# Kernel optimization log

Measured on AMD Instinct MI355X. Metric: run time of the kernel, lower is better.

Reference implementation:

```python
import jax, jax.numpy as jnp
import numpy as np

EMBED_DIM = 2048
NUM_HEADS = 32
NUM_KV_HEADS = 8
HEAD_DIM = EMBED_DIM // NUM_HEADS  # 64
KV_DIM = HEAD_DIM * NUM_KV_HEADS   # 512
ROPE_BASE = 10000.0


def rope_cos_sin(seq_len, dim):
    inv_freq = 1.0 / (ROPE_BASE ** (jnp.arange(0, dim, 2, dtype=jnp.float32) / dim))
    t = jnp.arange(seq_len, dtype=jnp.float32)
    freqs = jnp.outer(t, inv_freq)                 # [T, dim/2]
    emb = jnp.concatenate([freqs, freqs], axis=-1)  # [T, dim]
    return jnp.cos(emb), jnp.sin(emb)


def rotate_half(x):
    half = x.shape[-1] // 2
    return jnp.concatenate([-x[..., half:], x[..., :half]], axis=-1)


def setup_inputs() -> dict:
    key = jax.random.key(0)
    k_x, k_q, k_k, k_v, k_o = jax.random.split(key, 5)
    B, T, C = 2, 2048, EMBED_DIM
    s = 1.0 / np.sqrt(C)
    x = jax.random.normal(k_x, (B, T, C), dtype=jnp.float32)
    # Linear weights stored as [in, out]; no bias (bias=False)
    Wq = jax.random.normal(k_q, (C, EMBED_DIM), dtype=jnp.float32) * s
    Wk = jax.random.normal(k_k, (C, KV_DIM), dtype=jnp.float32) * s
    Wv = jax.random.normal(k_v, (C, KV_DIM), dtype=jnp.float32) * s
    Wo = jax.random.normal(k_o, (C, EMBED_DIM), dtype=jnp.float32) * s
    return {"x": x, "Wq": Wq, "Wk": Wk, "Wv": Wv, "Wo": Wo}


def reference(x, Wq, Wk, Wv, Wo):
    B, T, C = x.shape
    H, KVH, D = NUM_HEADS, NUM_KV_HEADS, HEAD_DIM
    scale = D ** -0.5
    rep = H // KVH

    q = (x @ Wq).reshape(B, T, H, D).transpose(0, 2, 1, 3)    # [B,H,T,D]
    k = (x @ Wk).reshape(B, T, KVH, D).transpose(0, 2, 1, 3)  # [B,KVH,T,D]
    v = (x @ Wv).reshape(B, T, KVH, D).transpose(0, 2, 1, 3)
    # repeat_interleave over head dim to expand KV heads
    k = jnp.repeat(k, rep, axis=1)  # [B,H,T,D]
    v = jnp.repeat(v, rep, axis=1)

    cos, sin = rope_cos_sin(T, D)
    cos = cos[None, None, :, :]
    sin = sin[None, None, :, :]
    q = q * cos + rotate_half(q) * sin
    k = k * cos + rotate_half(k) * sin

    att = jnp.einsum('bhtd,bhsd->bhts', q, k) * scale  # [B,H,T,T]
    att = jax.nn.softmax(att, axis=-1)                 # mask=None, dropout eval
    y = jnp.einsum('bhts,bhsd->bhtd', att, v)          # [B,H,T,D]
    y = y.transpose(0, 2, 1, 3).reshape(B, T, C)
    return y @ Wo
```

## Files before the change

kernel.cpp:

```cpp
#include <hip/hip_runtime.h>
#include <stdint.h>

#define Tn   2048
#define Cn   2048
#define Hn   32
#define KVHn 8
#define Dn   64
#define MR   4096
#define NQKV 3072
#define KD   2048

typedef __attribute__((ext_vector_type(4))) float fx4;
typedef __attribute__((ext_vector_type(8))) short frag8;

#define MFMA(a,b,c) __builtin_amdgcn_mfma_f32_16x16x32_bf16((a),(b),(c),0,0,0)

struct __align__(16) U16x8 { unsigned short s[8]; };

__device__ __forceinline__ unsigned short f2bf(float x){
  union { float f; unsigned u; } v; v.f = x;
  return (unsigned short)((v.u + 0x7FFFu + ((v.u >> 16) & 1u)) >> 16);
}
__device__ __forceinline__ float bf2f(unsigned short h){
  union { unsigned u; float f; } v; v.u = ((unsigned)h) << 16; return v.f;
}
__device__ __forceinline__ float sexp2(float x){
#if __has_builtin(__builtin_amdgcn_exp2f)
  return __builtin_amdgcn_exp2f(x);
#else
  return exp2f(x);
#endif
}
__device__ __forceinline__ unsigned cvtpk(float a, float b){
  unsigned r; asm("v_cvt_pk_bf16_f32 %0, %1, %2" : "=v"(r) : "v"(a), "v"(b)); return r;
}

typedef const __attribute__((address_space(1))) void cas1_void;
typedef __attribute__((address_space(3))) void as3_void;
__device__ __forceinline__ void gld16(const void* g, void* l){
  __builtin_amdgcn_global_load_lds((cas1_void*)g, (as3_void*)l, 16, 0, 0);
}

__global__ __launch_bounds__(256) void k_prep(const float* __restrict__ x, unsigned short* __restrict__ xb,
                                              const float* __restrict__ Wq, const float* __restrict__ Wk,
                                              const float* __restrict__ Wv, unsigned short* __restrict__ wqkvt,
                                              const float* __restrict__ Wo, unsigned short* __restrict__ wot,
                                              float2* __restrict__ cs){
  __shared__ float tile[64][65];
  int blk = blockIdx.x, t = threadIdx.x;
  if (blk < 2048) {
    size_t blockbase = (size_t)blk * 4096;
    #pragma unroll
    for (int j = 0; j < 4; ++j) {
      size_t i = blockbase + j * 1024 + t * 4;
      float4 v = *(const float4*)(x + i);
      ushort4 o; o.x = f2bf(v.x); o.y = f2bf(v.y); o.z = f2bf(v.z); o.w = f2bf(v.w);
      *(ushort4*)(xb + i) = o;
    }
    return;
  }
  if (blk >= 4608) {
    int i = (blk - 4608) * 256 + t;
    int tp = i >> 5, d = i & 31;
    float inv = powf(10000.0f, -(float)d * (1.0f/32.0f));
    float fr = (float)tp * inv;
    cs[i] = make_float2(cosf(fr), sinf(fr));
    return;
  }
  const float* src; int col0, ld, n0, k0; unsigned short* outp;
  if (blk < 3584) {
    int bx = blk - 2048; n0 = (bx % 48) * 64; k0 = (bx / 48) * 64; outp = wqkvt;
    if (n0 < 2048)      { src = Wq; col0 = n0;        ld = 2048; }
    else if (n0 < 2560) { src = Wk; col0 = n0 - 2048; ld = 512;  }
    else                { src = Wv; col0 = n0 - 2560; ld = 512;  }
  } else {
    int bx = blk - 3584; n0 = (bx % 32) * 64; k0 = (bx / 32) * 64; outp = wot;
    src = Wo; col0 = n0; ld = 2048;
  }
  int r = t >> 2, cc = (t & 3) << 4;
  const float* p = src + (size_t)(k0 + r) * ld + col0 + cc;
  #pragma unroll
  for (int j = 0; j < 16; j += 4) {
    float4 v = *(const float4*)(p + j);
    tile[r][cc + j + 0] = v.x; tile[r][cc + j + 1] = v.y;
    tile[r][cc + j + 2] = v.z; tile[r][cc + j + 3] = v.w;
  }
  __syncthreads();
  int n = t >> 2, kc = (t & 3) << 4;
  unsigned short* q = outp + (size_t)(n0 + n) * 2048 + k0 + kc;
  U16x8 o0, o1;
  #pragma unroll
  for (int j = 0; j < 8; ++j) o0.s[j] = f2bf(tile[kc + j][n]);
  #pragma unroll
  for (int j = 0; j < 8; ++j) o1.s[j] = f2bf(tile[kc + 8 + j][n]);
  *(U16x8*)(q) = o0;
  *(U16x8*)(q + 8) = o1;
}

template<int MODE>
__global__ __launch_bounds__(256) void k_gemm(const unsigned short* __restrict__ A,
                                              const unsigned short* __restrict__ Bt,
                                              void* __restrict__ Cp,
                                              int M, int N, int K,
                                              const float2* __restrict__ cs){
  __shared__ unsigned short As[128 * 64];
  __shared__ unsigned short Bs[128 * 64];
  int tid = threadIdx.x;
  int m0 = blockIdx.y * 128, n0 = blockIdx.x * 128;
  int w = tid >> 6, ln = tid & 63, lr = ln & 15, lg = ln >> 4;
  int wm = (w >> 1) * 64, wn = (w & 1) * 64;
  fx4 acc[4][4];
  #pragma unroll
  for (int i = 0; i < 4; ++i)
    #pragma unroll
    for (int j = 0; j < 4; ++j) acc[i][j] = (fx4){0.f,0.f,0.f,0.f};
  int steps = K >> 6;
  for (int kt = 0; kt < steps; ++kt) {
    int kb = kt << 6;
    #pragma unroll
    for (int it = 0; it < 4; ++it) {
      int nch = it * 256 + tid;
      int r = nch >> 3, c = (nch & 7) ^ (r & 7);
      gld16(A  + (size_t)(m0 + r) * K + kb + c * 8, (char*)As + nch * 16);
      gld16(Bt + (size_t)(n0 + r) * K + kb + c * 8, (char*)Bs + nch * 16);
    }
    __syncthreads();
    frag8 aF[4][2], bF[4][2];
    #pragma unroll
    for (int i = 0; i < 4; ++i) {
      int ra = wm + i * 16 + lr;
      int rb = wn + i * 16 + lr;
      #pragma unroll
      for (int kk = 0; kk < 2; ++kk) {
        aF[i][kk] = *(const frag8*)((const char*)As + ra * 128 + (((lg + 4*kk) ^ (ra & 7)) << 4));
        bF[i][kk] = *(const frag8*)((const char*)Bs + rb * 128 + (((lg + 4*kk) ^ (rb & 7)) << 4));
      }
    }
    #pragma unroll
    for (int kk = 0; kk < 2; ++kk)
      #pragma unroll
      for (int i = 0; i < 4; ++i)
        #pragma unroll
        for (int j = 0; j < 4; ++j)
          acc[i][j] = MFMA(aF[i][kk], bF[j][kk], acc[i][j]);
    __syncthreads();
  }
  if (MODE == 0) {
    #pragma unroll
    for (int i = 0; i < 4; ++i) {
      int row = m0 + wm + i * 16 + lg * 4;
      #pragma unroll
      for (int j = 0; j < 4; ++j) {
        int col = n0 + wn + j * 16 + lr;
        #pragma unroll
        for (int rr = 0; rr < 4; ++rr)
          ((float*)Cp)[(size_t)(row + rr) * N + col] = acc[i][j][rr];
      }
    }
  } else {
    int nb = n0 + wn;
    unsigned short* outp = (unsigned short*)Cp;
    if (nb < 2560) {
      float sc = (n0 < 2048) ? 0.180336880f : 1.0f;
      #pragma unroll
      for (int i = 0; i < 4; ++i) {
        int rowb = m0 + wm + i * 16 + lg * 4;
        #pragma unroll
        for (int jp = 0; jp < 2; ++jp) {
          int dA = jp * 16 + lr;
          #pragma unroll
          for (int rr = 0; rr < 4; ++rr) {
            int row = rowb + rr;
            float2 cv = cs[((row & (Tn-1)) << 5) + dA];
            float a = acc[i][jp][rr], b = acc[i][jp + 2][rr];
            outp[(size_t)row * N + nb + dA]      = f2bf((a * cv.x - b * cv.y) * sc);
            outp[(size_t)row * N + nb + dA + 32] = f2bf((b * cv.x + a * cv.y) * sc);
          }
        }
      }
    } else {
      #pragma unroll
      for (int i = 0; i < 4; ++i) {
        int row = m0 + wm + i * 16 + lg * 4;
        #pragma unroll
        for (int j = 0; j < 4; ++j) {
          int col = nb + j * 16 + lr;
          #pragma unroll
          for (int rr = 0; rr < 4; ++rr)
            outp[(size_t)(row + rr) * N + col] = f2bf(acc[i][j][rr]);
        }
      }
    }
  }
}

__global__ __launch_bounds__(256) void k_vt(const unsigned short* __restrict__ qkv,
                                            unsigned short* __restrict__ vt){
  __shared__ unsigned short tl[64][66];
  int head = blockIdx.y;
  int b = head >> 3, kvh = head & 7;
  int t0 = blockIdx.x * 64;
  int t = threadIdx.x;
  int r = t >> 2, cc = (t & 3) << 4;
  const unsigned short* p = qkv + (size_t)(b * Tn + t0 + r) * NQKV + 2560 + kvh * 64 + cc;
  U16x8 v0 = *(const U16x8*)(p);
  U16x8 v1 = *(const U16x8*)(p + 8);
  #pragma unroll
  for (int j = 0; j < 8; ++j) { tl[r][cc + j] = v0.s[j]; tl[r][cc + 8 + j] = v1.s[j]; }
  __syncthreads();
  int d = t >> 2, cpair = t & 3;
  unsigned short* q = vt + ((size_t)head * 64 + d) * Tn + t0;
  #pragma unroll
  for (int ci = 0; ci < 2; ++ci) {
    int c = cpair * 2 + ci;
    U16x8 oo;
    #pragma unroll
    for (int e = 0; e < 8; ++e)
      oo.s[e] = tl[32 * (c >> 2) + 16 * (e >> 2) + 4 * (c & 3) + (e & 3)][d];
    *(U16x8*)(q + c * 8) = oo;
  }
}

__global__ __launch_bounds__(512) void k_attn(const unsigned short* __restrict__ qkv,
                                              const unsigned short* __restrict__ vt,
                                              unsigned short* __restrict__ y){
  __shared__ unsigned short Ks[4][64 * 64];
  __shared__ unsigned short Vs[4][64 * 64];
  int tid = threadIdx.x, w = tid >> 6, ln = tid & 63, lq = ln & 15, lg = ln >> 4;
  int bh = blockIdx.y, b = bh >> 5, h = bh & 31, kvh = h >> 2;
  int q0 = blockIdx.x * 256;
  frag8 qF[2][2];
  #pragma unroll
  for (int s = 0; s < 2; ++s) {
    const unsigned short* qrow = qkv + (size_t)(b * Tn + q0 + w * 32 + 16 * s + lq) * NQKV + h * 64;
    qF[s][0] = *(const frag8*)(qrow + lg * 8);
    qF[s][1] = *(const frag8*)(qrow + 32 + lg * 8);
  }
  fx4 zero4 = (fx4){0.f, 0.f, 0.f, 0.f};
  asm volatile("" : "+v"(zero4));
  int n0 = tid;
  int r0 = n0 >> 3, c0 = (n0 & 7) ^ (r0 & 7);
  const unsigned short* kp0 = qkv + (size_t)b * Tn * NQKV + 2048 + kvh * 64 + (size_t)r0 * NQKV + c0 * 8;
  const unsigned short* vp0 = vt + ((size_t)(b * 8 + kvh) * 64 + r0) * Tn + c0 * 8;
  int koff0 = lq * 128 + (((lg)     ^ (lq & 7)) << 4);
  int koff1 = lq * 128 + (((lg + 4) ^ (lq & 7)) << 4);

#define STAGE(BUF) do {                                      \
    gld16(kp0, (char*)&Ks[BUF][0] + n0 * 16);                \
    gld16(vp0, (char*)&Vs[BUF][0] + n0 * 16);                \
    kp0 += 64 * NQKV; vp0 += 64;                             \
  } while (0)

#define PB(S, KK) ({ union { unsigned u[4]; frag8 f; } t_;                        \
    t_.u[0] = pu[S][2*(KK)][0]; t_.u[1] = pu[S][2*(KK)][1];                       \
    t_.u[2] = pu[S][2*(KK)+1][0]; t_.u[3] = pu[S][2*(KK)+1][1]; t_.f; })

#define PVSTEP(VF) do {                                                           \
    _Pragma("unroll")                                                             \
    for (int s = 0; s < 2; ++s)                                                   \
      _Pragma("unroll")                                                           \
      for (int df = 0; df < 4; ++df) {                                            \
        o[s][df] = MFMA(VF[df][0], PB(s, 0), o[s][df]);                           \
        o[s][df] = MFMA(VF[df][1], PB(s, 1), o[s][df]);                           \
      }                                                                           \
  } while (0)

#define TILE(BUF, VFCUR, VFPREV) do {                                             \
    const char* kb_ = (const char*)&Ks[BUF][0];                                   \
    const char* vb_ = (const char*)&Vs[BUF][0];                                   \
    frag8 kf[4][2];                                                               \
    _Pragma("unroll")                                                             \
    for (int mf = 0; mf < 4; ++mf) {                                              \
      kf[mf][0] = *(const frag8*)(kb_ + mf * 2048 + koff0);                       \
      kf[mf][1] = *(const frag8*)(kb_ + mf * 2048 + koff1);                       \
    }                                                                             \
    _Pragma("unroll")                                                             \
    for (int df = 0; df < 4; ++df) {                                              \
      VFCUR[df][0] = *(const frag8*)(vb_ + df * 2048 + koff0);                    \
      VFCUR[df][1] = *(const frag8*)(vb_ + df * 2048 + koff1);                    \
    }                                                                             \
    __builtin_amdgcn_s_setprio(1);                                                \
    PVSTEP(VFPREV);                       \
    fx4 sf[2][4];                                                                 \
    _Pragma("unroll")                                                             \
    for (int s = 0; s < 2; ++s)                                                   \
      _Pragma("unroll")                                                           \
      for (int mf = 0; mf < 4; ++mf) {                                            \
        sf[s][mf] = MFMA(kf[mf][0], qF[s][0], zero4);                             \
        sf[s][mf] = MFMA(kf[mf][1], qF[s][1], sf[s][mf]);                         \
      }                                                                           \
    __builtin_amdgcn_s_setprio(0);                                                \
    _Pragma("unroll")                                \
    for (int s = 0; s < 2; ++s) {                                                 \
      float ps = 0.f;                                                             \
      _Pragma("unroll")                                                           \
      for (int mf = 0; mf < 4; ++mf) {                                            \
        float p0 = sexp2(sf[s][mf][0]);                                           \
        float p1 = sexp2(sf[s][mf][1]);                                           \
        float p2 = sexp2(sf[s][mf][2]);                                           \
        float p3 = sexp2(sf[s][mf][3]);                                           \
        ps += (p0 + p1) + (p2 + p3);                                              \
        pu[s][mf][0] = cvtpk(p0, p1);                                             \
        pu[s][mf][1] = cvtpk(p2, p3);                                             \
      }                                                                           \
      lpart[s] += ps;                                                             \
    }                                                                             \
  } while (0)

  fx4 o[2][4];
  float lpart[2] = {0.f, 0.f};
  unsigned pu[2][4][2];
  frag8 vfA[4][2], vfB[4][2];
  #pragma unroll
  for (int s = 0; s < 2; ++s) {
    #pragma unroll
    for (int i = 0; i < 4; ++i) o[s][i] = (fx4){0.f, 0.f, 0.f, 0.f};
    #pragma unroll
    for (int mf = 0; mf < 4; ++mf) { pu[s][mf][0] = 0u; pu[s][mf][1] = 0u; }
  }
  #pragma unroll
  for (int df = 0; df < 4; ++df) {
    vfA[df][0] = (frag8){0,0,0,0,0,0,0,0};
    vfA[df][1] = (frag8){0,0,0,0,0,0,0,0};
  }

  STAGE(0); STAGE(1);
  __syncthreads();
  for (int kt = 0; kt < 32; kt += 4) {
    if (kt + 2 < 32) { STAGE(2); STAGE(3); }
    TILE(0, vfB, vfA);
    TILE(1, vfA, vfB);
    __syncthreads();
    if (kt + 4 < 32) { STAGE(0); STAGE(1); }
    TILE(2, vfB, vfA);
    TILE(3, vfA, vfB);
    __syncthreads();
  }
  __builtin_amdgcn_s_setprio(1);
  PVSTEP(vfA);
  __builtin_amdgcn_s_setprio(0);
#undef STAGE
#undef TILE
#undef PVSTEP
#undef PB

  #pragma unroll
  for (int s = 0; s < 2; ++s) {
    lpart[s] += __shfl_xor(lpart[s], 16);
    lpart[s] += __shfl_xor(lpart[s], 32);
    float inv = 1.0f / lpart[s];
    unsigned short* yp = y + (size_t)(b * Tn + q0 + w * 32 + 16 * s + lq) * Cn + h * 64;
    #pragma unroll
    for (int df = 0; df < 4; ++df) {
      unsigned lo = cvtpk(o[s][df][0] * inv, o[s][df][1] * inv);
      unsigned hi = cvtpk(o[s][df][2] * inv, o[s][df][3] * inv);
      *(uint2*)(yp + df * 16 + lg * 4) = make_uint2(lo, hi);
    }
  }
}

extern "C" void kernel_launch(void* const* d_in, const int* in_sizes, int n_in,
                              void* d_out, int out_size, void* d_ws, size_t ws_size,
                              hipStream_t stream){
  const float* x  = (const float*)d_in[0];
  const float* Wq = (const float*)d_in[1];
  const float* Wk = (const float*)d_in[2];
  const float* Wv = (const float*)d_in[3];
  const float* Wo = (const float*)d_in[4];
  char* ws = (char*)d_ws;
  size_t off = 0;
  unsigned short* xb    = (unsigned short*)(ws + off); off += (size_t)MR * KD * 2;
  unsigned short* wqkvt = (unsigned short*)(ws + off); off += (size_t)NQKV * KD * 2;
  unsigned short* wot   = (unsigned short*)(ws + off); off += (size_t)KD * KD * 2;
  unsigned short* qkv   = (unsigned short*)(ws + off); off += (size_t)MR * NQKV * 2;
  unsigned short* vtb   = (unsigned short*)(ws + off); off += (size_t)16 * 64 * Tn * 2;
  float2* cstab = (float2*)(ws + off); off += (size_t)Tn * 32 * 8;
  unsigned short* yb = xb;

  k_prep<<<4864, 256, 0, stream>>>(x, xb, Wq, Wk, Wv, wqkvt, Wo, wot, cstab);
  k_gemm<2><<<dim3(NQKV / 128, MR / 128), 256, 0, stream>>>(xb, wqkvt, qkv, MR, NQKV, KD, cstab);
  k_vt<<<dim3(Tn / 64, 16), 256, 0, stream>>>(qkv, vtb);
  k_attn<<<dim3(Tn / 256, 64), 512, 0, stream>>>(qkv, vtb, yb);
  k_gemm<0><<<dim3(KD / 128, MR / 128), 256, 0, stream>>>(yb, wot, d_out, MR, KD, KD, nullptr);
}
```

Measured before the change: 201.4 us.

## Replace QKV GEMM with 256x256-tile 8-wave kernel using phased double-buffered LDS

Adds a dedicated QKV projection GEMM that uses 256x256 output tiles, 512 threads and 8 waves, each wave computing a 128x64 sub-tile. K-chunks are split into halves and staged through a double-buffered LDS with global loads interleaved between MFMA phases, gated by explicit vmcnt waits and barriers. The goal is higher operand reuse per LDS load and better overlap of memory with compute than the previous 128x128 tile kernel. The RoPE/scale epilogue is kept. The costs are a large accumulator register footprint and only 192 blocks in the grid, which may underfill the device.

```diff
diff --git a/kernel.cpp b/kernel.cpp
--- a/kernel.cpp
+++ b/kernel.cpp
@@ -157,38 +157,127 @@
           ((float*)Cp)[(size_t)(row + rr) * N + col] = acc[i][j][rr];
       }
     }
-  } else {
-    int nb = n0 + wn;
-    unsigned short* outp = (unsigned short*)Cp;
-    if (nb < 2560) {
-      float sc = (n0 < 2048) ? 0.180336880f : 1.0f;
+  }
+}
+
+#define G8K 2048
+#define G8N 3072
+__global__ __launch_bounds__(512, 2) void k_gemm8(const unsigned short* __restrict__ A,
+                                                  const unsigned short* __restrict__ Bt,
+                                                  unsigned short* __restrict__ qkv,
+                                                  const float2* __restrict__ cs){
+  __shared__ unsigned short AS[2][2][8192];
+  __shared__ unsigned short BS[2][2][8192];
+  int tid = threadIdx.x;
+  int w = tid >> 6, ln = tid & 63, lr = ln & 15, lg = ln >> 4;
+  int wm = w >> 2, wn = w & 3;
+  int m0 = blockIdx.y * 256, n0 = blockIdx.x * 256;
+  int r0 = tid >> 2, c0 = (tid & 3) ^ (r0 & 3);
+  const unsigned short* srcA = A  + (size_t)(m0 + r0) * G8K + c0 * 8;
+  const unsigned short* srcB = Bt + (size_t)(n0 + r0) * G8K + c0 * 8;
+  int dstoff = tid * 16;
+  int foff = lr * 64 + ((lg ^ (lr & 3)) << 4);
+  int aw = wm * 8192;
+  int bw = wn * 4096;
+
+#define STGA8(DU, UU, T) do {                                                  \
+    const unsigned short* s_ = srcA + (size_t)(T) * 64 + (UU) * 32;            \
+    char* d_ = (char*)&AS[DU][UU][0] + dstoff;                                 \
+    gld16(s_, d_);                                                             \
+    gld16(s_ + (size_t)128 * G8K, d_ + 8192);                                  \
+  } while (0)
+#define STGB8(DU, UU, T) do {                                                  \
+    const unsigned short* s_ = srcB + (size_t)(T) * 64 + (UU) * 32;            \
+    char* d_ = (char*)&BS[DU][UU][0] + dstoff;                                 \
+    gld16(s_, d_);                                                             \
+    gld16(s_ + (size_t)128 * G8K, d_ + 8192);                                  \
+  } while (0)
+#define BAR8() __builtin_amdgcn_s_barrier()
+#define VMC8(n) asm volatile("s_waitcnt vmcnt(" #n ")" ::: "memory")
+
+#define PHASE8(DU, UU, I0, LOADB_, STGSTMT, VM4) do {                          \
+    frag8 aF_[4];                                                              \
+    _Pragma("unroll")                                                          \
+    for (int ii = 0; ii < 4; ++ii)                                             \
+      aF_[ii] = *(const frag8*)((const char*)&AS[DU][UU][0] + aw + ((I0)+ii) * 1024 + foff); \
+    if (LOADB_) {                                                              \
+      _Pragma("unroll")                                                        \
+      for (int jj = 0; jj < 4; ++jj)                                           \
+        bF[jj] = *(const frag8*)((const char*)&BS[DU][UU][0] + bw + jj * 1024 + foff); \
+    }                                                                          \
+    STGSTMT;                                                                   \
+    if (VM4) VMC8(4);                                                          \
+    BAR8();                                                                    \
+    __builtin_amdgcn_s_setprio(1);                                             \
+    _Pragma("unroll")                                                          \
+    for (int ii = 0; ii < 4; ++ii)                                             \
+      _Pragma("unroll")                                                        \
+      for (int jj = 0; jj < 4; ++jj)                                           \
+        acc[(I0)+ii][jj] = MFMA(aF_[ii], bF[jj], acc[(I0)+ii][jj]);            \
+    __builtin_amdgcn_s_setprio(0);                                             \
+    BAR8();                                                                    \
+  } while (0)
+
+  fx4 acc[8][4];
+  #pragma unroll
+  for (int i = 0; i < 8; ++i)
+    #pragma unroll
+    for (int j = 0; j < 4; ++j) acc[i][j] = (fx4){0.f,0.f,0.f,0.f};
+  frag8 bF[4];
+
+  STGA8(0,0,0); STGB8(0,0,0); STGA8(0,1,0); STGB8(0,1,0); STGA8(1,0,1); STGB8(1,0,1);
+  VMC8(0);
+  BAR8();
+
+  for (int it2 = 0; it2 < 16; ++it2) {
+    int t1 = 2*it2 + 1;
+    int t2 = (2*it2 + 2 < 32) ? 2*it2 + 2 : 31;
+    int t3 = (2*it2 + 3 < 32) ? 2*it2 + 3 : 31;
+    PHASE8(0,0, 0, 1, STGA8(1,1,t1), 0);
+    PHASE8(0,0, 4, 0, STGB8(1,1,t1), 0);
+    PHASE8(0,1, 0, 1, STGA8(0,0,t2), 0);
+    PHASE8(0,1, 4, 0, STGB8(0,0,t2), 1);
+    PHASE8(1,0, 0, 1, STGA8(0,1,t2), 0);
+    PHASE8(1,0, 4, 0, STGB8(0,1,t2), 0);
+    PHASE8(1,1, 0, 1, STGA8(1,0,t3), 0);
+    PHASE8(1,1, 4, 0, STGB8(1,0,t3), 1);
+  }
+  VMC8(0);
+#undef PHASE8
+#undef STGA8
+#undef STGB8
+#undef BAR8
+#undef VMC8
+
+  int nb = n0 + wn * 64;
+  if (nb < 2560) {
+    float sc = (nb < 2048) ? 0.180336880f : 1.0f;
+    #pragma unroll
+    for (int i = 0; i < 8; ++i) {
+      int rowb = m0 + wm * 128 + i * 16 + lg * 4;
       #pragma unroll
-      for (int i = 0; i < 4; ++i) {
-        int rowb = m0 + wm + i * 16 + lg * 4;
+      for (int jp = 0; jp < 2; ++jp) {
+        int dA = jp * 16 + lr;
         #pragma unroll
-        for (int jp = 0; jp < 2; ++jp) {
-          int dA = jp * 16 + lr;
-          #pragma unroll
-          for (int rr = 0; rr < 4; ++rr) {
-            int row = rowb + rr;
-            float2 cv = cs[((row & (Tn-1)) << 5) + dA];
-            float a = acc[i][jp][rr], b = acc[i][jp + 2][rr];
-            outp[(size_t)row * N + nb + dA]      = f2bf((a * cv.x - b * cv.y) * sc);
-            outp[(size_t)row * N + nb + dA + 32] = f2bf((b * cv.x + a * cv.y) * sc);
-          }
+        for (int rr = 0; rr < 4; ++rr) {
+          int row = rowb + rr;
+          float2 cv = cs[((row & (Tn-1)) << 5) + dA];
+          float a = acc[i][jp][rr], b = acc[i][jp + 2][rr];
+          qkv[(size_t)row * G8N + nb + dA]      = f2bf((a * cv.x - b * cv.y) * sc);
+          qkv[(size_t)row * G8N + nb + dA + 32] = f2bf((b * cv.x + a * cv.y) * sc);
         }
       }
-    } else {
+    }
+  } else {
+    #pragma unroll
+    for (int i = 0; i < 8; ++i) {
+      int rowb = m0 + wm * 128 + i * 16 + lg * 4;
       #pragma unroll
-      for (int i = 0; i < 4; ++i) {
-        int row = m0 + wm + i * 16 + lg * 4;
+      for (int j = 0; j < 4; ++j) {
+        int col = nb + j * 16 + lr;
         #pragma unroll
-        for (int j = 0; j < 4; ++j) {
-          int col = nb + j * 16 + lr;
-          #pragma unroll
-          for (int rr = 0; rr < 4; ++rr)
-            outp[(size_t)(row + rr) * N + col] = f2bf(acc[i][j][rr]);
-        }
+        for (int rr = 0; rr < 4; ++rr)
+          qkv[(size_t)(rowb + rr) * G8N + col] = f2bf(acc[i][j][rr]);
       }
     }
   }
@@ -280,7 +369,7 @@
       VFCUR[df][1] = *(const frag8*)(vb_ + df * 2048 + koff1);                    \
     }                                                                             \
     __builtin_amdgcn_s_setprio(1);                                                \
-    PVSTEP(VFPREV);                       \
+    PVSTEP(VFPREV);                                                               \
     fx4 sf[2][4];                                                                 \
     _Pragma("unroll")                                                             \
     for (int s = 0; s < 2; ++s)                                                   \
@@ -290,7 +379,7 @@
         sf[s][mf] = MFMA(kf[mf][1], qF[s][1], sf[s][mf]);                         \
       }                                                                           \
     __builtin_amdgcn_s_setprio(0);                                                \
-    _Pragma("unroll")                                \
+    _Pragma("unroll")                                                             \
     for (int s = 0; s < 2; ++s) {                                                 \
       float ps = 0.f;                                                             \
       _Pragma("unroll")                                                           \
@@ -378,7 +467,7 @@
   unsigned short* yb = xb;
 
   k_prep<<<4864, 256, 0, stream>>>(x, xb, Wq, Wk, Wv, wqkvt, Wo, wot, cstab);
-  k_gemm<2><<<dim3(NQKV / 128, MR / 128), 256, 0, stream>>>(xb, wqkvt, qkv, MR, NQKV, KD, cstab);
+  k_gemm8<<<dim3(G8N / 256, MR / 256), 512, 0, stream>>>(xb, wqkvt, qkv, cstab);
   k_vt<<<dim3(Tn / 64, 16), 256, 0, stream>>>(qkv, vtb);
   k_attn<<<dim3(Tn / 256, 64), 512, 0, stream>>>(qkv, vtb, yb);
   k_gemm<0><<<dim3(KD / 128, MR / 128), 256, 0, stream>>>(yb, wot, d_out, MR, KD, KD, nullptr);
```

Result: no change. 204.2 us (+1.4%).
